# Kernel optimization log

Hardware: AMD Instinct MI355X
Metric: run time of the kernel (lower is better)

Reference implementation:

```python
import jax, jax.numpy as jnp
import numpy as np


def setup_inputs() -> dict:
    key = jax.random.key(0)
    k1, k2 = jax.random.split(key)
    B, T, F, H = 32, 2048, 400, 1152
    x = jax.random.normal(k1, (B, T, F), dtype=jnp.float32)
    # fused gate weights (F*kernel_window, 3*H); small init like keras 'uniform'
    W = jax.random.normal(k2, (2 * F, 3 * H), dtype=jnp.float32) * 0.05
    b = jnp.zeros((3 * H,), dtype=jnp.float32)
    h0 = jnp.zeros((B, H), dtype=jnp.float32)
    return {"x": x, "W": W, "b": b, "h0": h0}


def reference(x, W, b, h0):
    """QRNN with 'fo' pooling, kernel_window=2, keep_fastai_bug=True, inference.

    Per timestep (as in QRNNCell_.call):
      merged_t = [x_t, x_{t-1}]                      (x_{-1} = 0)
      z, f, o  = split(merged_t @ W + b, 3)
      z = tanh(z); f = sigmoid(f); o = sigmoid(o)
      h_t = z*f + (1-f)*h_{t-1}   (fastai-bug variant; h is carried state)
      c_t = o*h_t                 (cell output at step t)
    Returns the full output sequence c: [B, T, H].
    """
    B, T, F = x.shape
    # previous-timestep inputs (kernel_window=2): shift right, zero-pad t=0
    x_prev = jnp.concatenate([jnp.zeros((B, 1, F), x.dtype), x[:, :-1]], axis=1)
    merged = jnp.concatenate([x, x_prev], axis=-1)            # [B, T, 2F]
    logits = jnp.einsum('btf,fg->btg', merged, W) + b          # [B, T, 3H]
    z, f, o = jnp.split(logits, 3, axis=-1)
    z = jnp.tanh(z)
    f = jax.nn.sigmoid(f)
    o = jax.nn.sigmoid(o)

    def step(h_prev, gates):
        zt, ft, ot = gates
        h_t = zt * ft + (1.0 - ft) * h_prev
        return h_t, ot * h_t

    # scan over time: [T, B, H]
    _, c = jax.lax.scan(step, h0,
                        (z.transpose(1, 0, 2), f.transpose(1, 0, 2), o.transpose(1, 0, 2)))
    return c.transpose(1, 0, 2)                                # [B, T, H]
```

## Files before the change

### kernel.cpp

```cpp
#include <hip/hip_runtime.h>

#define BB 32
#define TT 2048
#define FF 400
#define HH 1152
#define MM 65536
#define NN 3456
#define KK 800
#define MT2 256
#define NT 27
#define KTL 25
#define CH 64
#define CL 32

typedef __attribute__((ext_vector_type(8))) short short8;
typedef __attribute__((ext_vector_type(4))) float f32x4;
typedef _Float16 hx4 __attribute__((ext_vector_type(4)));
typedef float f2 __attribute__((ext_vector_type(2)));

__device__ __forceinline__ unsigned short f2bf(float f) {
  union { float f; unsigned u; } v; v.f = f;
  unsigned r = v.u + 0x7FFFu + ((v.u >> 16) & 1u);
  return (unsigned short)(r >> 16);
}

__device__ __forceinline__ size_t quadOff(int mt, int ntS, int wr, int wc,
                                          int mr, int nr, int kg, int l15) {
  return ((((size_t)(mt * 9 + ntS) * 2 + wr) * 2 + wc) * 32 + mr * 4 + nr) * 256
         + (size_t)(kg * 16 + l15) * 4;
}

__global__ __launch_bounds__(256) void pack_W_k(const float* __restrict__ W,
                                                unsigned short* __restrict__ Wws) {
  const int nt = blockIdx.x, kt = blockIdx.y;
  for (int c = threadIdx.x; c < 512; c += 256) {
    const int kg = c >> 7, n = c & 127;
    const int g = nt * 128 + n;
    const int k0 = kt * 32 + kg * 8;
    short8 o;
#pragma unroll
    for (int j = 0; j < 8; ++j) o[j] = (short)f2bf(W[(size_t)(k0 + j) * NN + g]);
    *(short8*)(Wws + ((size_t)(nt * KTL + kt) * 512 + c) * 8) = o;
  }
}

__global__ __launch_bounds__(256) void pack_A_k(const float* __restrict__ x,
                                                unsigned short* __restrict__ Aws) {
  const int mt = blockIdx.x, kt = blockIdx.y;
  for (int c = threadIdx.x; c < 1024; c += 256) {
    const int kg = c >> 8, mm = c & 255;
    const int m = mt * 256 + mm;
    const int b = m >> 11, t = m & 2047;
    const int k = kt * 32 + kg * 8;
    short8 o;
    const float* src = nullptr;
    if (k < FF) src = x + (size_t)(b * TT + t) * FF + k;
    else if (t > 0) src = x + (size_t)(b * TT + t - 1) * FF + (k - FF);
    if (src) {
      f32x4 v0 = *(const f32x4*)(src);
      f32x4 v1 = *(const f32x4*)(src + 4);
#pragma unroll
      for (int j = 0; j < 4; ++j) o[j] = (short)f2bf(v0[j]);
#pragma unroll
      for (int j = 0; j < 4; ++j) o[4 + j] = (short)f2bf(v1[j]);
    } else {
#pragma unroll
      for (int j = 0; j < 8; ++j) o[j] = 0;
    }
    *(short8*)(Aws + ((size_t)(mt * KTL + kt) * 1024 + c) * 8) = o;
  }
}

__global__ __launch_bounds__(256, 2) void gemm_k(const unsigned short* __restrict__ Aws,
                                                 const unsigned short* __restrict__ Wws,
                                                 const float* __restrict__ bias,
                                                 _Float16* __restrict__ Zh,
                                                 _Float16* __restrict__ Fh,
                                                 _Float16* __restrict__ Oh) {
  const int bid = blockIdx.x;
  const int xcd = bid & 7;
  const int local = bid >> 3;
  const int ng = local / 288;
  const int r0 = local - ng * 288;
  const int mtl = r0 / 9;
  const int nti = r0 - mtl * 9;
  const int mt = xcd * 32 + mtl;
  const int nt = ng * 9 + nti;

  const int tid = threadIdx.x;
  const int lane = tid & 63, w = tid >> 6;
  const int wr = w >> 1, wc = w & 1;
  const int l15 = lane & 15, kg = lane >> 4;

  const unsigned short* ga = Aws + (size_t)mt * KTL * 8192
                             + (size_t)(kg * 256 + wr * 128 + l15) * 8;
  const unsigned short* gb = Wws + (size_t)nt * KTL * 4096
                             + (size_t)(kg * 128 + wc * 64 + l15) * 8;

  f32x4 acc[8][4] = {};
  short8 a0[8], b0[4], a1[8], b1[4];

#define LOADT(AF, BF, tt)                                                    \
  do {                                                                       \
    const unsigned short* _a = ga + (size_t)(tt) * 8192;                     \
    const unsigned short* _b = gb + (size_t)(tt) * 4096;                     \
    _Pragma("unroll")                                                        \
    for (int mr = 0; mr < 8; ++mr) AF[mr] = *(const short8*)(_a + mr * 128); \
    _Pragma("unroll")                                                        \
    for (int nr = 0; nr < 4; ++nr) BF[nr] = *(const short8*)(_b + nr * 128); \
  } while (0)

#define MFMAC(AF, BF)                                                              \
  do {                                                                             \
    __builtin_amdgcn_s_setprio(1);                                                 \
    _Pragma("unroll")                                                              \
    for (int mr = 0; mr < 8; ++mr)                                                 \
      _Pragma("unroll")                                                            \
      for (int nr = 0; nr < 4; ++nr)                                               \
        acc[mr][nr] = __builtin_amdgcn_mfma_f32_16x16x32_bf16(AF[mr], BF[nr],      \
                                                              acc[mr][nr], 0, 0, 0); \
    __builtin_amdgcn_s_setprio(0);                                                 \
  } while (0)

  LOADT(a0, b0, 0);
  LOADT(a1, b1, 1);

#pragma unroll 1
  for (int t = 0; t < KTL - 1; t += 2) {
    MFMAC(a0, b0);
    if (t + 2 < KTL) LOADT(a0, b0, t + 2);
    MFMAC(a1, b1);
    if (t + 3 < KTL) LOADT(a1, b1, t + 3);
  }
  MFMAC(a0, b0);

#undef LOADT
#undef MFMAC

  const int sector = ng;
  const int ntS = nti;
  _Float16* __restrict__ dst = (sector == 0) ? Zh : ((sector == 1) ? Fh : Oh);
  const int gbase = nt * 128 + wc * 64 + l15;
  const size_t wavebase = (((size_t)(mt * 9 + ntS) * 2 + wr) * 2 + wc) * 8192 + (size_t)lane * 4;
#pragma unroll
  for (int nr = 0; nr < 4; ++nr) {
    const float bv = bias[gbase + nr * 16];
#pragma unroll
    for (int mr = 0; mr < 8; ++mr) {
      f32x4 v = acc[mr][nr];
      hx4 hv;
#pragma unroll
      for (int rr = 0; rr < 4; ++rr) {
        float xv = v[rr] + bv;
        float s;
        if (sector == 0) {
          float e = __expf(2.0f * xv);
          s = 1.0f - 2.0f / (e + 1.0f);
        } else {
          s = 1.0f / (1.0f + __expf(-xv));
        }
        hv[rr] = (_Float16)s;
      }
      __builtin_nontemporal_store(hv, (hx4*)(dst + wavebase + (size_t)(mr * 4 + nr) * 256));
    }
  }
}

__global__ __launch_bounds__(256) void scan1_k(const _Float16* __restrict__ Zh,
                                               const _Float16* __restrict__ Fh,
                                               f2* __restrict__ PQ) {
  const int bid = blockIdx.x;
  const int b = bid / 288;
  const int rem = bid - b * 288;
  const int hb = rem >> 5, cp = rem & 31;
  const int tid = threadIdx.x;
  const int hloc = tid & 127, sub = tid >> 7;
  const int ch = cp * 2 + sub;
  const int ntS = hb, wc = hloc >> 6, nr = (hloc >> 4) & 3, l15 = hloc & 15;
  const int tm = ch >> 3, wr = (ch >> 2) & 1, mrh = ch & 3;
  const int mt = b * 8 + tm;

  float P = 1.f, Q = 0.f;
#pragma unroll
  for (int mi = 0; mi < 2; ++mi) {
#pragma unroll
    for (int kg = 0; kg < 4; ++kg) {
      const size_t off = quadOff(mt, ntS, wr, wc, mrh * 2 + mi, nr, kg, l15);
      hx4 z = __builtin_nontemporal_load((const hx4*)(Zh + off));
      hx4 f = __builtin_nontemporal_load((const hx4*)(Fh + off));
#pragma unroll
      for (int s = 0; s < 4; ++s) {
        float fv = (float)f[s], a = 1.f - fv;
        P *= a;
        Q = a * Q + fv * (float)z[s];
      }
    }
  }
  f2 o; o[0] = P; o[1] = Q;
  PQ[((size_t)b * CH + ch) * HH + hb * 128 + hloc] = o;
}

__global__ __launch_bounds__(256) void scan2_k(const f2* __restrict__ PQ,
                                               const float* __restrict__ h0,
                                               float* __restrict__ Hs) {
  const int idx = blockIdx.x * 256 + threadIdx.x;
  const int b = idx / HH, h = idx - b * HH;
  float cur = h0[b * HH + h];
#pragma unroll 4
  for (int c = 0; c < CH; ++c) {
    Hs[((size_t)b * CH + c) * HH + h] = cur;
    f2 pq = PQ[((size_t)b * CH + c) * HH + h];
    cur = pq[0] * cur + pq[1];
  }
}

__global__ __launch_bounds__(256) void scan3_k(const _Float16* __restrict__ Zh,
                                               const _Float16* __restrict__ Fh,
                                               const _Float16* __restrict__ Oh,
                                               const float* __restrict__ Hs,
                                               float* __restrict__ Out) {
  __shared__ float buf[64 * 132];
  const int bid = blockIdx.x;
  const int b = bid / 288;
  const int rem = bid - b * 288;
  const int hb = rem >> 5, cp = rem & 31;
  const int tid = threadIdx.x;
  const int hloc = tid & 127, sub = tid >> 7;
  const int ch = cp * 2 + sub;
  const int h = hb * 128 + hloc;
  const int ntS = hb, wc = hloc >> 6, nr = (hloc >> 4) & 3, l15 = hloc & 15;
  const int tm = ch >> 3, wr = (ch >> 2) & 1, mrh = ch & 3;
  const int mt = b * 8 + tm;

  float hcur = Hs[((size_t)b * CH + ch) * HH + h];
#pragma unroll
  for (int mi = 0; mi < 2; ++mi) {
#pragma unroll
    for (int kg = 0; kg < 4; ++kg) {
      const size_t off = quadOff(mt, ntS, wr, wc, mrh * 2 + mi, nr, kg, l15);
      hx4 z = __builtin_nontemporal_load((const hx4*)(Zh + off));
      hx4 f = __builtin_nontemporal_load((const hx4*)(Fh + off));
      hx4 o = __builtin_nontemporal_load((const hx4*)(Oh + off));
#pragma unroll
      for (int s = 0; s < 4; ++s) {
        hcur = fmaf((float)f[s], (float)z[s] - hcur, hcur);
        buf[(sub * 32 + mi * 16 + kg * 4 + s) * 132 + hloc] = (float)o[s] * hcur;
      }
    }
  }
  __syncthreads();
  const int lane32 = tid & 31, grp = tid >> 5;
  float* outb = Out + (size_t)(b * TT + cp * 64) * HH + hb * 128 + lane32 * 4;
#pragma unroll
  for (int rr = 0; rr < 8; ++rr) {
    const int row = grp * 8 + rr;
    f32x4 v = *(const f32x4*)&buf[row * 132 + lane32 * 4];
    __builtin_nontemporal_store(v, (f32x4*)(outb + (size_t)row * HH));
  }
}

extern "C" void kernel_launch(void* const* d_in, const int* in_sizes, int n_in,
                              void* d_out, int out_size, void* d_ws, size_t ws_size,
                              hipStream_t stream) {
  const float* x    = (const float*)d_in[0];
  const float* W    = (const float*)d_in[1];
  const float* bias = (const float*)d_in[2];
  const float* h0   = (const float*)d_in[3];
  float* Out = (float*)d_out;
  char* ws = (char*)d_ws;

  const size_t A_BYTES  = (size_t)MT2 * KTL * 16384;
  const size_t W_BYTES  = (size_t)NT * KTL * 8192;
  const size_t G_BYTES  = (size_t)MM * HH * 2;
  const size_t PQ_BYTES = (size_t)BB * CH * HH * 8;
  unsigned short* Aws = (unsigned short*)ws;
  unsigned short* Wws = (unsigned short*)(ws + A_BYTES);
  _Float16* Zh = (_Float16*)(ws + A_BYTES + W_BYTES);
  _Float16* Fh = (_Float16*)(ws + A_BYTES + W_BYTES + G_BYTES);
  _Float16* Oh = (_Float16*)(ws + A_BYTES + W_BYTES + 2 * G_BYTES);
  f2* PQ = (f2*)(ws + A_BYTES + W_BYTES + 3 * G_BYTES);
  float* Hs = (float*)(ws + A_BYTES + W_BYTES + 3 * G_BYTES + PQ_BYTES);
  (void)ws_size; (void)in_sizes; (void)n_in; (void)out_size;

  pack_W_k<<<dim3(NT, KTL), 256, 0, stream>>>(W, Wws);
  pack_A_k<<<dim3(MT2, KTL), 256, 0, stream>>>(x, Aws);
  gemm_k<<<MT2 * NT, 256, 0, stream>>>(Aws, Wws, bias, Zh, Fh, Oh);
  scan1_k<<<BB * 9 * 32, 256, 0, stream>>>(Zh, Fh, PQ);
  scan2_k<<<BB * HH / 256, 256, 0, stream>>>(PQ, h0, Hs);
  scan3_k<<<BB * 9 * 32, 256, 0, stream>>>(Zh, Fh, Oh, Hs, Out);
}
```

Baseline: 616.6 us.

## Switch GEMM to 32x32x16 bf16 MFMA and remap gate intermediate layout

```diff
diff --git a/kernel.cpp b/kernel.cpp
--- a/kernel.cpp
+++ b/kernel.cpp
@@ -15,6 +15,7 @@
 
 typedef __attribute__((ext_vector_type(8))) short short8;
 typedef __attribute__((ext_vector_type(4))) float f32x4;
+typedef __attribute__((ext_vector_type(16))) float f32x16;
 typedef _Float16 hx4 __attribute__((ext_vector_type(4)));
 typedef float f2 __attribute__((ext_vector_type(2)));
 
@@ -24,10 +25,11 @@
   return (unsigned short)(r >> 16);
 }
 
-__device__ __forceinline__ size_t quadOff(int mt, int ntS, int wr, int wc,
-                                          int mr, int nr, int kg, int l15) {
-  return ((((size_t)(mt * 9 + ntS) * 2 + wr) * 2 + wc) * 32 + mr * 4 + nr) * 256
-         + (size_t)(kg * 16 + l15) * 4;
+__device__ __forceinline__ size_t qOff(int mt, int ntS, int wr, int wc,
+                                       int mb, int nb, int q, int hi, int l31) {
+  return ((size_t)((mt * 9 + ntS) * 4 + wr * 2 + wc)) * 8192
+         + (size_t)(((mb * 2 + nb) * 4 + q) * 256)
+         + (size_t)((hi * 32 + l31) * 4);
 }
 
 __global__ __launch_bounds__(256) void pack_W_k(const float* __restrict__ W,
@@ -90,36 +92,44 @@
   const int tid = threadIdx.x;
   const int lane = tid & 63, w = tid >> 6;
   const int wr = w >> 1, wc = w & 1;
-  const int l15 = lane & 15, kg = lane >> 4;
+  const int l31 = lane & 31, hi = lane >> 5;
 
   const unsigned short* ga = Aws + (size_t)mt * KTL * 8192
-                             + (size_t)(kg * 256 + wr * 128 + l15) * 8;
+                             + (size_t)hi * 2048 + (size_t)(wr * 128 + l31) * 8;
   const unsigned short* gb = Wws + (size_t)nt * KTL * 4096
-                             + (size_t)(kg * 128 + wc * 64 + l15) * 8;
-
-  f32x4 acc[8][4] = {};
+                             + (size_t)hi * 1024 + (size_t)(wc * 64 + l31) * 8;
+
+  f32x16 acc[4][2] = {};
   short8 a0[8], b0[4], a1[8], b1[4];
 
-#define LOADT(AF, BF, tt)                                                    \
-  do {                                                                       \
-    const unsigned short* _a = ga + (size_t)(tt) * 8192;                     \
-    const unsigned short* _b = gb + (size_t)(tt) * 4096;                     \
-    _Pragma("unroll")                                                        \
-    for (int mr = 0; mr < 8; ++mr) AF[mr] = *(const short8*)(_a + mr * 128); \
-    _Pragma("unroll")                                                        \
-    for (int nr = 0; nr < 4; ++nr) BF[nr] = *(const short8*)(_b + nr * 128); \
+#define LOADT(AF, BF, tt)                                                     \
+  do {                                                                        \
+    const unsigned short* _a = ga + (size_t)(tt) * 8192;                      \
+    const unsigned short* _b = gb + (size_t)(tt) * 4096;                      \
+    _Pragma("unroll")                                                         \
+    for (int mb = 0; mb < 4; ++mb)                                            \
+      _Pragma("unroll")                                                       \
+      for (int ks = 0; ks < 2; ++ks)                                          \
+        AF[mb * 2 + ks] = *(const short8*)(_a + ks * 4096 + mb * 256);        \
+    _Pragma("unroll")                                                         \
+    for (int nb = 0; nb < 2; ++nb)                                            \
+      _Pragma("unroll")                                                       \
+      for (int ks = 0; ks < 2; ++ks)                                          \
+        BF[nb * 2 + ks] = *(const short8*)(_b + ks * 2048 + nb * 256);        \
   } while (0)
 
-#define MFMAC(AF, BF)                                                              \
-  do {                                                                             \
-    __builtin_amdgcn_s_setprio(1);                                                 \
-    _Pragma("unroll")                                                              \
-    for (int mr = 0; mr < 8; ++mr)                                                 \
-      _Pragma("unroll")                                                            \
-      for (int nr = 0; nr < 4; ++nr)                                               \
-        acc[mr][nr] = __builtin_amdgcn_mfma_f32_16x16x32_bf16(AF[mr], BF[nr],      \
-                                                              acc[mr][nr], 0, 0, 0); \
-    __builtin_amdgcn_s_setprio(0);                                                 \
+#define MFMAC(AF, BF)                                                               \
+  do {                                                                              \
+    __builtin_amdgcn_s_setprio(1);                                                  \
+    _Pragma("unroll")                                                               \
+    for (int ks = 0; ks < 2; ++ks)                                                  \
+      _Pragma("unroll")                                                             \
+      for (int mb = 0; mb < 4; ++mb)                                                \
+        _Pragma("unroll")                                                           \
+        for (int nb = 0; nb < 2; ++nb)                                              \
+          acc[mb][nb] = __builtin_amdgcn_mfma_f32_32x32x16_bf16(                    \
+              AF[mb * 2 + ks], BF[nb * 2 + ks], acc[mb][nb], 0, 0, 0);              \
+    __builtin_amdgcn_s_setprio(0);                                                  \
   } while (0)
 
   LOADT(a0, b0, 0);
@@ -140,28 +150,33 @@
   const int sector = ng;
   const int ntS = nti;
   _Float16* __restrict__ dst = (sector == 0) ? Zh : ((sector == 1) ? Fh : Oh);
-  const int gbase = nt * 128 + wc * 64 + l15;
-  const size_t wavebase = (((size_t)(mt * 9 + ntS) * 2 + wr) * 2 + wc) * 8192 + (size_t)lane * 4;
-#pragma unroll
-  for (int nr = 0; nr < 4; ++nr) {
-    const float bv = bias[gbase + nr * 16];
-#pragma unroll
-    for (int mr = 0; mr < 8; ++mr) {
-      f32x4 v = acc[mr][nr];
-      hx4 hv;
-#pragma unroll
-      for (int rr = 0; rr < 4; ++rr) {
-        float xv = v[rr] + bv;
-        float s;
-        if (sector == 0) {
-          float e = __expf(2.0f * xv);
-          s = 1.0f - 2.0f / (e + 1.0f);
-        } else {
-          s = 1.0f / (1.0f + __expf(-xv));
+  const int hbase = nt * 128 + wc * 64 + l31;
+  const size_t wavebase = ((size_t)((mt * 9 + ntS) * 4 + wr * 2 + wc)) * 8192
+                          + (size_t)((hi * 32 + l31) * 4);
+#pragma unroll
+  for (int mb = 0; mb < 4; ++mb) {
+#pragma unroll
+    for (int nb = 0; nb < 2; ++nb) {
+      const float bv = bias[hbase + nb * 32];
+      f32x16 v = acc[mb][nb];
+#pragma unroll
+      for (int q = 0; q < 4; ++q) {
+        hx4 hv;
+#pragma unroll
+        for (int rr = 0; rr < 4; ++rr) {
+          float xv = v[q * 4 + rr] + bv;
+          float s;
+          if (sector == 0) {
+            float e = __expf(2.0f * xv);
+            s = 1.0f - 2.0f / (e + 1.0f);
+          } else {
+            s = 1.0f / (1.0f + __expf(-xv));
+          }
+          hv[rr] = (_Float16)s;
         }
-        hv[rr] = (_Float16)s;
+        __builtin_nontemporal_store(hv,
+            (hx4*)(dst + wavebase + (size_t)(((mb * 2 + nb) * 4 + q) * 256)));
       }
-      __builtin_nontemporal_store(hv, (hx4*)(dst + wavebase + (size_t)(mr * 4 + nr) * 256));
     }
   }
 }
@@ -176,16 +191,16 @@
   const int tid = threadIdx.x;
   const int hloc = tid & 127, sub = tid >> 7;
   const int ch = cp * 2 + sub;
-  const int ntS = hb, wc = hloc >> 6, nr = (hloc >> 4) & 3, l15 = hloc & 15;
-  const int tm = ch >> 3, wr = (ch >> 2) & 1, mrh = ch & 3;
+  const int wc = hloc >> 6, nb = (hloc >> 5) & 1, l31 = hloc & 31;
+  const int tm = ch >> 3, wr = (ch >> 2) & 1, mb = ch & 3;
   const int mt = b * 8 + tm;
 
   float P = 1.f, Q = 0.f;
 #pragma unroll
-  for (int mi = 0; mi < 2; ++mi) {
-#pragma unroll
-    for (int kg = 0; kg < 4; ++kg) {
-      const size_t off = quadOff(mt, ntS, wr, wc, mrh * 2 + mi, nr, kg, l15);
+  for (int q = 0; q < 4; ++q) {
+#pragma unroll
+    for (int hi = 0; hi < 2; ++hi) {
+      const size_t off = qOff(mt, hb, wr, wc, mb, nb, q, hi, l31);
       hx4 z = __builtin_nontemporal_load((const hx4*)(Zh + off));
       hx4 f = __builtin_nontemporal_load((const hx4*)(Fh + off));
 #pragma unroll
@@ -228,23 +243,23 @@
   const int hloc = tid & 127, sub = tid >> 7;
   const int ch = cp * 2 + sub;
   const int h = hb * 128 + hloc;
-  const int ntS = hb, wc = hloc >> 6, nr = (hloc >> 4) & 3, l15 = hloc & 15;
-  const int tm = ch >> 3, wr = (ch >> 2) & 1, mrh = ch & 3;
+  const int wc = hloc >> 6, nb = (hloc >> 5) & 1, l31 = hloc & 31;
+  const int tm = ch >> 3, wr = (ch >> 2) & 1, mb = ch & 3;
   const int mt = b * 8 + tm;
 
   float hcur = Hs[((size_t)b * CH + ch) * HH + h];
 #pragma unroll
-  for (int mi = 0; mi < 2; ++mi) {
-#pragma unroll
-    for (int kg = 0; kg < 4; ++kg) {
-      const size_t off = quadOff(mt, ntS, wr, wc, mrh * 2 + mi, nr, kg, l15);
+  for (int q = 0; q < 4; ++q) {
+#pragma unroll
+    for (int hi = 0; hi < 2; ++hi) {
+      const size_t off = qOff(mt, hb, wr, wc, mb, nb, q, hi, l31);
       hx4 z = __builtin_nontemporal_load((const hx4*)(Zh + off));
       hx4 f = __builtin_nontemporal_load((const hx4*)(Fh + off));
       hx4 o = __builtin_nontemporal_load((const hx4*)(Oh + off));
 #pragma unroll
       for (int s = 0; s < 4; ++s) {
         hcur = fmaf((float)f[s], (float)z[s] - hcur, hcur);
-        buf[(sub * 32 + mi * 16 + kg * 4 + s) * 132 + hloc] = (float)o[s] * hcur;
+        buf[(sub * 32 + q * 8 + hi * 4 + s) * 132 + hloc] = (float)o[s] * hcur;
       }
     }
   }
```

New measurement: 698.7 us. 13.3% more time.
